# Kernel optimization log

Hardware: AMD Instinct MI355X
Metric: run time of the kernel (lower is better)

Reference implementation:

```python
import jax, jax.numpy as jnp
import numpy as np

H = 256
NUM_REL = 480
NUM_ENT = 23000
N_TRIPLES = 8192
T = 10  # cur_ts == path_len window


def _lin_params(key, din, dout):
    kw, _ = jax.random.split(key)
    W = jax.random.normal(kw, (din, dout), dtype=jnp.float32) * 0.02
    b = jnp.zeros((dout,), dtype=jnp.float32)
    return W, b


def setup_inputs() -> dict:
    key = jax.random.key(0)
    ks = jax.random.split(key, 16)
    pre_emb = jax.random.normal(ks[0], (NUM_ENT, H), dtype=jnp.float32)
    r_emb = jax.random.normal(ks[1], (NUM_REL, H), dtype=jnp.float32)
    # history counts: sparse non-negative (zeros are masked to -1e9 in softmax)
    part = jax.random.uniform(ks[2], (N_TRIPLES, T * NUM_REL), dtype=jnp.float32)
    mask = jax.random.uniform(ks[3], (N_TRIPLES, T * NUM_REL)) < 0.3
    partial_embeding = jnp.where(mask, part, 0.0)
    sub_idx = jax.random.randint(ks[4], (N_TRIPLES,), 0, NUM_ENT)
    rel_idx = jax.random.randint(ks[5], (N_TRIPLES,), 0, NUM_REL)
    obj_idx = jax.random.randint(ks[6], (N_TRIPLES,), 0, NUM_ENT)
    Wm1, bm1 = _lin_params(ks[7], H, 2 * H)
    Wm2, bm2 = _lin_params(ks[8], 2 * H, H)
    Wattn, battn = _lin_params(ks[9], H, H)
    Wh1, bh1 = _lin_params(ks[10], H, H)
    Wh2, bh2 = _lin_params(ks[11], H, H)
    Walign, balign = _lin_params(ks[12], H, H)
    Wih = jax.random.normal(ks[13], (H, 3 * H), dtype=jnp.float32) * 0.02
    Whh = jax.random.normal(ks[14], (H, 3 * H), dtype=jnp.float32) * 0.02
    bih = jnp.zeros((3 * H,), dtype=jnp.float32)
    bhh = jnp.zeros((3 * H,), dtype=jnp.float32)
    return dict(pre_emb=pre_emb, r_emb=r_emb, partial_embeding=partial_embeding,
                sub_idx=sub_idx, rel_idx=rel_idx, obj_idx=obj_idx, cur_ts=T,
                Wm1=Wm1, bm1=bm1, Wm2=Wm2, bm2=bm2, Wattn=Wattn, battn=battn,
                Wh1=Wh1, bh1=bh1, Wh2=Wh2, bh2=bh2, Walign=Walign, balign=balign,
                Wih=Wih, Whh=Whh, bih=bih, bhh=bhh)


def _gru_cell(x, h, Wih, Whh, bih, bhh):
    # torch.nn.GRUCell math
    gi = x @ Wih + bih
    gh = h @ Whh + bhh
    i_r, i_z, i_n = jnp.split(gi, 3, axis=-1)
    h_r, h_z, h_n = jnp.split(gh, 3, axis=-1)
    r = jax.nn.sigmoid(i_r + h_r)
    z = jax.nn.sigmoid(i_z + h_z)
    n = jnp.tanh(i_n + r * h_n)
    return (1.0 - z) * n + z * h


def reference(pre_emb, r_emb, partial_embeding, sub_idx, rel_idx, obj_idx, cur_ts,
              Wm1, bm1, Wm2, bm2, Wattn, battn, Wh1, bh1, Wh2, bh2,
              Walign, balign, Wih, Whh, bih, bhh):
    n = partial_embeding.shape[0]
    num_rel = r_emb.shape[0]
    t = cur_ts  # path window covers [0, cur_ts)
    # relation mapping
    mapped_rel = (r_emb @ Wm1 + bm1) @ Wm2 + bm2            # [R, H]
    q_rel = mapped_rel[rel_idx]                               # [N, H]
    # attention logits base (loop-invariant): q W_attn mapped_rel^T
    base = (q_rel @ Wattn + battn) @ mapped_rel.T            # [N, R]
    # [N, t*R] -> [t, N, R] time-major slices
    hist = partial_embeding[:, : t * num_rel].reshape(n, t, num_rel).swapaxes(0, 1)
    h0 = jnp.zeros((n, mapped_rel.shape[1]), dtype=pre_emb.dtype)

    def step(h, cur):
        attn = cur * base
        attn = jax.nn.softmax(jnp.where(attn == 0, -1e9, attn), axis=1)
        x = attn @ mapped_rel                                 # [N, H]
        return _gru_cell(x, h, Wih, Whh, bih, bhh), None

    gru_hidden, _ = jax.lax.scan(step, h0, hist)
    # predicted history + match loss
    predicted_hist = 0.1 * ((q_rel @ Wh1 + bh1) @ Wh2 + bh2) + q_rel
    match_loss = jnp.mean((predicted_hist - gru_hidden) ** 2)
    # forward_forth (distmult)
    h2 = _gru_cell(q_rel, predicted_hist, Wih, Whh, bih, bhh)  # [N, H]
    sub = pre_emb[sub_idx]
    score_ = ((sub @ Walign + balign) * h2) @ (pre_emb @ Walign + balign).T  # [N, E]
    # BCE(sigmoid(score_), one_hot(obj)): per-elem -y*logsig(s) - (1-y)*logsig(-s)
    pos = score_[jnp.arange(n), obj_idx]
    path_loss = (-jnp.sum(jax.nn.log_sigmoid(-score_)) - jnp.sum(pos)) / (score_.size)
    score = jax.nn.sigmoid(score_)
    return match_loss, path_loss, score
```

## Files before the change

kernel.cpp:

```cpp
#include <hip/hip_runtime.h>
#include <hip/hip_bf16.h>
#include <stdint.h>

#define DEV __device__ __forceinline__

typedef unsigned short u16;
typedef __attribute__((ext_vector_type(8))) short bf16x8;
typedef __attribute__((ext_vector_type(4))) float f32x4;
typedef __attribute__((ext_vector_type(4))) unsigned short u16x4;

constexpr int H  = 256;
constexpr int R  = 480;
constexpr int RP = 512;
constexpr int NE = 23000;
constexpr int NT = 8192;
constexpr int TT = 10;

DEV u16 f2b(float f) {
  union { float f; unsigned u; } x; x.f = f;
  unsigned u = x.u;
  return (u16)((u + 0x7fffu + ((u >> 16) & 1u)) >> 16);
}
DEV float b2f(u16 h) {
  union { unsigned u; float f; } x; x.u = ((unsigned)h) << 16;
  return x.f;
}

DEV void gload_lds16(const u16* g, u16* lds) {
  __builtin_amdgcn_global_load_lds(
      (const __attribute__((address_space(1))) unsigned int*)g,
      (__attribute__((address_space(3))) unsigned int*)lds, 16, 0, 0);
}

__launch_bounds__(256)
__global__ void stageA_k(const float* __restrict__ r_emb,
                         const float* __restrict__ Wm1, const float* __restrict__ bm1,
                         const float* __restrict__ Wm2, const float* __restrict__ bm2,
                         const float* __restrict__ Wattn, const float* __restrict__ battn,
                         const float* __restrict__ Wih,
                         const float* __restrict__ Wh1, const float* __restrict__ bh1,
                         const float* __restrict__ Wh2, const float* __restrict__ bh2,
                         const float* __restrict__ Whh, const float* __restrict__ bhh,
                         const float* __restrict__ bih, const float* __restrict__ Walign,
                         float* __restrict__ mapped, float* __restrict__ t1,
                         float* __restrict__ Pg, float* __restrict__ G2,
                         u16* __restrict__ MWT, u16* __restrict__ WhhT,
                         u16* __restrict__ WalignT, float* __restrict__ bsum) {
  const int j = threadIdx.x;
  if (blockIdx.x >= 480) {
    const int b = blockIdx.x - 480;
    if (b < 768) {
      WhhT[(size_t)b * 256 + j] = f2b(Whh[(size_t)j * 768 + b]);
    } else if (b < 1024) {
      const int n = b - 768;
      WalignT[(size_t)n * 256 + j] = f2b(Walign[(size_t)j * 256 + n]);
    } else if (b < 1027) {
      const int c = (b - 1024) * 256 + j;
      if (c < 768) bsum[c] = bih[c] + (c < 512 ? bhh[c] : 0.f);
    } else {
      const int row = (b - 1027) * 256 + j;
      if (row < 768) {
        const u16x4 z = {0, 0, 0, 0};
        #pragma unroll
        for (int c = 480; c < 512; c += 4) *(u16x4*)&MWT[(size_t)row * RP + c] = z;
      }
    }
    return;
  }
  __shared__ float re[256], hid[512], mp[256], p1l[256], Pl[256];
  __shared__ float mwl[768], pwl[768];
  __shared__ f32x4 red4[256];
  const int r = blockIdx.x;
  const f32x4 z4 = {0.f, 0.f, 0.f, 0.f};
  re[j] = r_emb[(size_t)r * 256 + j];
  __syncthreads();
  {
    const int q = j & 127, g = j >> 7;
    f32x4 acc = (g == 0) ? *(const f32x4*)&bm1[q * 4] : z4;
    for (int k = g * 128; k < g * 128 + 128; ++k)
      acc += re[k] * *(const f32x4*)&Wm1[(size_t)k * 512 + q * 4];
    red4[j] = acc;
    __syncthreads();
    if (j < 128) *(f32x4*)&hid[j * 4] = red4[j] + red4[j + 128];
    __syncthreads();
  }
  {
    const int q = j & 63, g = j >> 6;
    f32x4 acc = (g == 0) ? *(const f32x4*)&bm2[q * 4] : z4;
    for (int k = g * 128; k < g * 128 + 128; ++k)
      acc += hid[k] * *(const f32x4*)&Wm2[(size_t)k * 256 + q * 4];
    red4[j] = acc;
    __syncthreads();
    if (j < 64) {
      const f32x4 s = red4[j] + red4[j + 64] + red4[j + 128] + red4[j + 192];
      *(f32x4*)&mp[j * 4] = s;
      *(f32x4*)&mapped[(size_t)r * 256 + j * 4] = s;
    }
    __syncthreads();
  }
  {
    const int q = j & 63, g = j >> 6;
    f32x4 acc = (g == 0) ? *(const f32x4*)&battn[q * 4] : z4;
    for (int k = g * 64; k < g * 64 + 64; ++k)
      acc += mp[k] * *(const f32x4*)&Wattn[(size_t)k * 256 + q * 4];
    red4[j] = acc;
    __syncthreads();
    if (j < 64)
      *(f32x4*)&t1[(size_t)r * 256 + j * 4] =
          red4[j] + red4[j + 64] + red4[j + 128] + red4[j + 192];
    __syncthreads();
  }
  if (j < 192) {
    f32x4 acc = z4;
    for (int k = 0; k < 256; ++k)
      acc += mp[k] * *(const f32x4*)&Wih[(size_t)k * 768 + j * 4];
    *(f32x4*)&mwl[j * 4] = acc;
    #pragma unroll
    for (int c = 0; c < 4; ++c) MWT[(size_t)(j * 4 + c) * RP + r] = f2b(acc[c]);
  }
  __syncthreads();
  {
    const int q = j & 63, g = j >> 6;
    f32x4 acc = (g == 0) ? *(const f32x4*)&bh1[q * 4] : z4;
    for (int k = g * 64; k < g * 64 + 64; ++k)
      acc += mp[k] * *(const f32x4*)&Wh1[(size_t)k * 256 + q * 4];
    red4[j] = acc;
    __syncthreads();
    if (j < 64) *(f32x4*)&p1l[j * 4] = red4[j] + red4[j + 64] + red4[j + 128] + red4[j + 192];
    __syncthreads();
  }
  {
    const int q = j & 63, g = j >> 6;
    f32x4 acc = (g == 0) ? *(const f32x4*)&bh2[q * 4] : z4;
    for (int k = g * 64; k < g * 64 + 64; ++k)
      acc += p1l[k] * *(const f32x4*)&Wh2[(size_t)k * 256 + q * 4];
    red4[j] = acc;
    __syncthreads();
    if (j < 64) {
      f32x4 s = red4[j] + red4[j + 64] + red4[j + 128] + red4[j + 192];
      const f32x4 mv = *(const f32x4*)&mp[j * 4];
      #pragma unroll
      for (int c = 0; c < 4; ++c) s[c] = 0.1f * s[c] + mv[c];
      *(f32x4*)&Pl[j * 4] = s;
      *(f32x4*)&Pg[(size_t)r * 256 + j * 4] = s;
    }
    __syncthreads();
  }
  if (j < 192) {
    f32x4 acc = *(const f32x4*)&bhh[j * 4];
    for (int k = 0; k < 256; ++k)
      acc += Pl[k] * *(const f32x4*)&Whh[(size_t)k * 768 + j * 4];
    *(f32x4*)&pwl[j * 4] = acc;
  }
  __syncthreads();
  {
    const float rg = 1.f / (1.f + __expf(-(mwl[j] + bih[j] + pwl[j])));
    const float zg = 1.f / (1.f + __expf(-(mwl[j + 256] + bih[j + 256] + pwl[j + 256])));
    const float ng = tanhf(mwl[j + 512] + bih[j + 512] + rg * pwl[j + 512]);
    G2[(size_t)r * 256 + j] = (1.f - zg) * ng + zg * Pl[j];
  }
}

__global__ void sgemm_bt_k(const float* __restrict__ A, const float* __restrict__ W,
                           float* __restrict__ C, int M, int N, int K) {
  const int idx = blockIdx.x * 256 + threadIdx.x;
  if (idx >= M * N) return;
  const int i = idx / N, j = idx % N;
  const f32x4* a4 = (const f32x4*)(A + (size_t)i * K);
  const f32x4* w4 = (const f32x4*)(W + (size_t)j * K);
  f32x4 acc = {0.f, 0.f, 0.f, 0.f};
  for (int k = 0; k < K / 4; ++k) acc += a4[k] * w4[k];
  C[idx] = acc[0] + acc[1] + acc[2] + acc[3];
}

__global__ void softmax_all_k(const float* __restrict__ part, const float* __restrict__ B480,
                              const int* __restrict__ rel_idx, u16* __restrict__ attn) {
  const int task = blockIdx.x * 4 + (threadIdx.x >> 6);
  const int lane = threadIdx.x & 63;
  const int tt = task >> 13;
  const int i  = task & (NT - 1);
  const float* cur = part + (size_t)i * (TT * R) + (size_t)tt * R;
  const float* b = B480 + (size_t)rel_idx[i] * R;
  f32x4 v[2];
  float m = -3e38f;
  const bool act1 = lane < 56;
  #pragma unroll
  for (int jj = 0; jj < 2; ++jj) {
    const int r0 = jj * 256 + lane * 4;
    f32x4 val = {-1e9f, -1e9f, -1e9f, -1e9f};
    if (jj == 0 || act1) {
      const f32x4 c4 = *(const f32x4*)&cur[r0];
      const f32x4 b4 = *(const f32x4*)&b[r0];
      #pragma unroll
      for (int x = 0; x < 4; ++x) {
        val[x] = (c4[x] == 0.f) ? -1e9f : c4[x] * b4[x];
        m = fmaxf(m, val[x]);
      }
    }
    v[jj] = val;
  }
  #pragma unroll
  for (int o = 32; o; o >>= 1) m = fmaxf(m, __shfl_xor(m, o));
  float s = 0.f;
  #pragma unroll
  for (int jj = 0; jj < 2; ++jj) {
    if (jj == 0 || act1) {
      #pragma unroll
      for (int x = 0; x < 4; ++x) { v[jj][x] = __expf(v[jj][x] - m); s += v[jj][x]; }
    }
  }
  #pragma unroll
  for (int o = 32; o; o >>= 1) s += __shfl_xor(s, o);
  const float inv = 1.f / s;
  u16* arow = attn + (size_t)task * RP;
  #pragma unroll
  for (int jj = 0; jj < 2; ++jj) {
    const int r0 = jj * 256 + lane * 4;
    u16x4 o = {0, 0, 0, 0};
    if (jj == 0 || act1) {
      #pragma unroll
      for (int x = 0; x < 4; ++x) o[x] = f2b(v[jj][x] * inv);
    }
    *(u16x4*)&arow[r0] = o;
  }
}

__launch_bounds__(256)
__global__ void scan_k(const u16* __restrict__ WhhT, const float* __restrict__ bhh,
                       const u16* __restrict__ gi_all, float* __restrict__ hbuf) {
  __shared__ __align__(16) u16 As[32 * 256];
  __shared__ __align__(16) u16 Bs[2][192 * 64];
  const int tid = threadIdx.x;
  const int lane = tid & 63;
  const int wv = tid >> 6;
  const int rf = wv >> 1;
  const int ch = wv & 1;
  const int fr = lane & 15;
  const int fq = lane >> 4;
  const int row_l = rf * 16 + fr;
  const int grow = blockIdx.x * 32 + row_l;
  const int sw = (fr & 7) * 8;

  auto stageB = [&](int buf, int cg, int k0) {
    #pragma unroll
    for (int it = 0; it < 6; ++it) {
      const int c = it * 256 + tid;
      const int vr = c >> 3, s = c & 7;
      const int vcol = ((vr >> 6) * 256) + cg * 64 + (vr & 63);
      gload_lds16(WhhT + (size_t)vcol * 256 + k0 + ((s ^ (vr & 7)) * 8),
                  &Bs[buf][(it * 256 + wv * 64) * 8]);
    }
  };

  float hreg[4][2][4];
  #pragma unroll
  for (int cg = 0; cg < 4; ++cg)
    #pragma unroll
    for (int nn = 0; nn < 2; ++nn)
      #pragma unroll
      for (int j = 0; j < 4; ++j) hreg[cg][nn][j] = 0.f;

  for (int t = 0; t < TT; ++t) {
    const u16* gi = gi_all + (size_t)t * NT * 768;
    #pragma unroll
    for (int cg = 0; cg < 4; ++cg) {
      f32x4 acc[6] = {};
      u16x4 gv[3][2];
      #pragma unroll
      for (int nn = 0; nn < 2; ++nn) {
        const int c = cg * 64 + ch * 32 + nn * 16 + fq * 4;
        const size_t gb = (size_t)grow * 768 + c;
        gv[0][nn] = *(const u16x4*)&gi[gb];
        gv[1][nn] = *(const u16x4*)&gi[gb + 256];
        gv[2][nn] = *(const u16x4*)&gi[gb + 512];
      }
      if (t > 0) {
        stageB(0, cg, 0);
        #pragma unroll
        for (int ki = 0; ki < 4; ++ki) {
          const int cb = ki & 1;
          if (ki < 3) {
            stageB(cb ^ 1, cg, (ki + 1) * 64);
            asm volatile("s_waitcnt vmcnt(6)" ::: "memory");
          } else {
            asm volatile("s_waitcnt vmcnt(0)" ::: "memory");
          }
          __builtin_amdgcn_sched_barrier(0);
          __builtin_amdgcn_s_barrier();
          #pragma unroll
          for (int kk = 0; kk < 2; ++kk) {
            const int ko = (ki * 64 + kk * 32 + fq * 8) ^ sw;
            const bf16x8 a = *(const bf16x8*)&As[row_l * 256 + ko];
            const int bo = (kk * 32 + fq * 8) ^ sw;
            #pragma unroll
            for (int g = 0; g < 3; ++g)
              #pragma unroll
              for (int nn = 0; nn < 2; ++nn) {
                const int vr = g * 64 + ch * 32 + nn * 16 + fr;
                const bf16x8 b = *(const bf16x8*)&Bs[cb][vr * 64 + bo];
                acc[g * 2 + nn] =
                    __builtin_amdgcn_mfma_f32_16x16x32_bf16(b, a, acc[g * 2 + nn], 0, 0, 0);
              }
          }
          __builtin_amdgcn_s_barrier();
        }
      }
      #pragma unroll
      for (int nn = 0; nn < 2; ++nn) {
        const int c = cg * 64 + ch * 32 + nn * 16 + fq * 4;
        const f32x4 bn = *(const f32x4*)&bhh[512 + c];
        #pragma unroll
        for (int j = 0; j < 4; ++j) {
          const float rg = 1.f / (1.f + __expf(-(b2f(gv[0][nn][j]) + acc[nn][j])));
          const float zg = 1.f / (1.f + __expf(-(b2f(gv[1][nn][j]) + acc[2 + nn][j])));
          const float ng = tanhf(b2f(gv[2][nn][j]) + rg * (acc[4 + nn][j] + bn[j]));
          hreg[cg][nn][j] = (1.f - zg) * ng + zg * hreg[cg][nn][j];
        }
      }
    }
    #pragma unroll
    for (int cg = 0; cg < 4; ++cg)
      #pragma unroll
      for (int nn = 0; nn < 2; ++nn) {
        const int c = cg * 64 + ch * 32 + nn * 16 + fq * 4;
        u16x4 o;
        #pragma unroll
        for (int j = 0; j < 4; ++j) o[j] = f2b(hreg[cg][nn][j]);
        *(u16x4*)&As[row_l * 256 + (c ^ sw)] = o;
        if (t == TT - 1) {
          f32x4 hv;
          #pragma unroll
          for (int j = 0; j < 4; ++j) hv[j] = hreg[cg][nn][j];
          *(f32x4*)&hbuf[(size_t)grow * 256 + c] = hv;
        }
      }
    __syncthreads();
  }
}

__global__ void gather_sub_k(const float* __restrict__ pre, const int* __restrict__ sub,
                             u16* __restrict__ sb) {
  const int q = blockIdx.x * 256 + threadIdx.x;
  const int i = q >> 6, c = (q & 63) * 4;
  const f32x4 v = *(const f32x4*)&pre[(size_t)sub[i] * H + c];
  u16x4 o;
  #pragma unroll
  for (int j = 0; j < 4; ++j) o[j] = f2b(v[j]);
  *(u16x4*)&sb[(size_t)q * 4] = o;
}
__global__ void cvt_pre_k(const float* __restrict__ pre, u16* __restrict__ pb) {
  const int q = blockIdx.x * 256 + threadIdx.x;
  const f32x4 v = *(const f32x4*)&pre[(size_t)q * 4];
  u16x4 o;
  #pragma unroll
  for (int j = 0; j < 4; ++j) o[j] = f2b(v[j]);
  *(u16x4*)&pb[(size_t)q * 4] = o;
}

__global__ void finalize_k(const float* __restrict__ mp, const float* __restrict__ sp,
                           float* __restrict__ out) {
  const int tid = threadIdx.x;
  float s1 = 0.f, s2 = 0.f;
  for (int i = tid; i < 128; i += 256) s1 += mp[i];
  for (int i = tid; i < 2880; i += 256) s2 += sp[i];
  #pragma unroll
  for (int o = 32; o; o >>= 1) {
    s1 += __shfl_down(s1, o); s2 += __shfl_down(s2, o);
  }
  __shared__ float r1[4], r2[4];
  if ((tid & 63) == 0) { r1[tid >> 6] = s1; r2[tid >> 6] = s2; }
  __syncthreads();
  if (tid == 0) {
    const float a = r1[0] + r1[1] + r1[2] + r1[3];
    const float b = r2[0] + r2[1] + r2[2] + r2[3];
    out[0] = a / 2097152.f;
    out[1] = b / 188416000.f;
  }
}

template <int MODE>
__launch_bounds__(256)
__global__ void gemm_k(const u16* __restrict__ A, const u16* __restrict__ Bt,
                       const float* __restrict__ bias,
                       float* __restrict__ Cf, u16* __restrict__ Cb,
                       int M, int N, int K,
                       float* __restrict__ out2, float* __restrict__ part,
                       const int* __restrict__ idxv, const float* __restrict__ Pf,
                       const float* __restrict__ G2f, const float* __restrict__ hf) {
  __shared__ __align__(16) u16 As[128 * 64];
  __shared__ __align__(16) u16 Bs[128 * 64];
  __shared__ float red[4];
  const int tid = threadIdx.x;
  const int lane = tid & 63;
  const int wv = tid >> 6;
  const int nbx = gridDim.x;
  int flat = blockIdx.y * nbx + blockIdx.x;
  const int nwg = nbx * gridDim.y;
  if ((nwg & 7) == 0) flat = (flat & 7) * (nwg >> 3) + (flat >> 3);
  const int bx = flat % nbx;
  const int by = flat / nbx;
  const int m0 = by * 128;
  const int n0 = bx * 128;
  const int wm = (wv >> 1) * 64;
  const int wn = (wv & 1) * 64;
  const int fr = lane & 15;
  const int fq = lane >> 4;
  const int sw = (lane & 7) * 8;
  f32x4 acc[4][4] = {};

  const int nsteps = K >> 6;
  for (int kt = 0; kt < nsteps; ++kt) {
    const int k0 = kt * 64;
    if (kt > 0) __syncthreads();
    #pragma unroll
    for (int it = 0; it < 4; ++it) {
      const int c = it * 256 + tid;
      const int row = c >> 3, s = c & 7;
      const int sc = (s ^ (row & 7)) * 8;
      int gr = m0 + row; gr = gr < M ? gr : M - 1;
      gload_lds16(A + (size_t)gr * K + k0 + sc, &As[(it * 256 + wv * 64) * 8]);
      int nr = n0 + row; nr = nr < N ? nr : N - 1;
      gload_lds16(Bt + (size_t)nr * K + k0 + sc, &Bs[(it * 256 + wv * 64) * 8]);
    }
    asm volatile("s_waitcnt vmcnt(0)" ::: "memory");
    __builtin_amdgcn_sched_barrier(0);
    __builtin_amdgcn_s_barrier();
    #pragma unroll
    for (int kk = 0; kk < 2; ++kk) {
      const int ko = (kk * 32 + fq * 8) ^ sw;
      bf16x8 a[4], b[4];
      #pragma unroll
      for (int mi = 0; mi < 4; ++mi)
        a[mi] = *(const bf16x8*)&As[(wm + mi * 16 + fr) * 64 + ko];
      #pragma unroll
      for (int ni = 0; ni < 4; ++ni)
        b[ni] = *(const bf16x8*)&Bs[(wn + ni * 16 + fr) * 64 + ko];
      #pragma unroll
      for (int mi = 0; mi < 4; ++mi)
        #pragma unroll
        for (int ni = 0; ni < 4; ++ni)
          acc[mi][ni] = __builtin_amdgcn_mfma_f32_16x16x32_bf16(b[ni], a[mi], acc[mi][ni], 0, 0, 0);
    }
  }

  float local = 0.f;
  #pragma unroll
  for (int mi = 0; mi < 4; ++mi) {
    const int rowm = m0 + wm + mi * 16 + fr;
    int iv = 0;
    if (MODE == 2) iv = idxv[rowm < M ? rowm : M - 1];
    #pragma unroll
    for (int ni = 0; ni < 4; ++ni) {
      const int col = n0 + wn + ni * 16 + fq * 4;
      if (rowm < M && col < N) {
        f32x4 v = acc[mi][ni];
        if (MODE == 0) {
          if (bias != nullptr) {
            const f32x4 bv = *(const f32x4*)&bias[col];
            #pragma unroll
            for (int j = 0; j < 4; ++j) v[j] += bv[j];
          }
          if (Cf) *(f32x4*)&Cf[(size_t)rowm * N + col] = v;
          if (Cb) {
            u16x4 o;
            #pragma unroll
            for (int j = 0; j < 4; ++j) o[j] = f2b(v[j]);
            *(u16x4*)&Cb[(size_t)rowm * N + col] = o;
          }
        } else {
          const f32x4 bv = *(const f32x4*)&bias[col];
          const f32x4 Pv = *(const f32x4*)&Pf[(size_t)iv * H + col];
          const f32x4 Gv = *(const f32x4*)&G2f[(size_t)iv * H + col];
          const f32x4 hv = *(const f32x4*)&hf[(size_t)rowm * H + col];
          u16x4 o;
          #pragma unroll
          for (int j = 0; j < 4; ++j) {
            const float d = Pv[j] - hv[j];
            local += d * d;
            o[j] = f2b((v[j] + bv[j]) * Gv[j]);
          }
          *(u16x4*)&Cb[(size_t)rowm * N + col] = o;
        }
      }
    }
  }
  if (MODE == 2) {
    #pragma unroll
    for (int o = 32; o; o >>= 1) local += __shfl_down(local, o);
    if (lane == 0) red[wv] = local;
    __syncthreads();
    if (tid == 0) part[blockIdx.y * gridDim.x + blockIdx.x] = red[0] + red[1] + red[2] + red[3];
  }
}

template <int MODE>
__launch_bounds__(512)
__global__ void gemm256_k(const u16* __restrict__ A, const u16* __restrict__ Bt,
                          const float* __restrict__ bias, u16* __restrict__ Cb,
                          int M, int N, int K,
                          float* __restrict__ out2, float* __restrict__ part,
                          const int* __restrict__ idxv) {
  __shared__ __align__(16) u16 As[256 * 64];
  __shared__ __align__(16) u16 Bs[256 * 64];
  __shared__ float red[8];
  const int tid = threadIdx.x;
  const int lane = tid & 63;
  const int wv = tid >> 6;
  const int nbx = gridDim.x;
  int flat = blockIdx.y * nbx + blockIdx.x;
  const int nwg = nbx * gridDim.y;
  if ((nwg & 7) == 0) flat = (flat & 7) * (nwg >> 3) + (flat >> 3);
  const int bx = flat % nbx;
  const int by = flat / nbx;
  const int m0 = by * 256;
  const int n0 = bx * 256;
  const int wm = (wv >> 2) * 128;
  const int wn = (wv & 3) * 64;
  const int fr = lane & 15;
  const int fq = lane >> 4;
  const int sw = (lane & 7) * 8;
  f32x4 acc[8][4] = {};

  const int nsteps = K >> 6;
  for (int kt = 0; kt < nsteps; ++kt) {
    const int k0 = kt * 64;
    if (kt > 0) __syncthreads();
    #pragma unroll
    for (int it = 0; it < 4; ++it) {
      const int c = it * 512 + tid;
      const int row = c >> 3, s = c & 7;
      const int sc = (s ^ (row & 7)) * 8;
      int gr = m0 + row; gr = gr < M ? gr : M - 1;
      gload_lds16(A + (size_t)gr * K + k0 + sc, &As[(it * 512 + wv * 64) * 8]);
      int nr = n0 + row; nr = nr < N ? nr : N - 1;
      gload_lds16(Bt + (size_t)nr * K + k0 + sc, &Bs[(it * 512 + wv * 64) * 8]);
    }
    asm volatile("s_waitcnt vmcnt(0)" ::: "memory");
    __builtin_amdgcn_sched_barrier(0);
    __builtin_amdgcn_s_barrier();
    #pragma unroll
    for (int kk = 0; kk < 2; ++kk) {
      const int ko = (kk * 32 + fq * 8) ^ sw;
      bf16x8 a[8], b[4];
      #pragma unroll
      for (int mi = 0; mi < 8; ++mi)
        a[mi] = *(const bf16x8*)&As[(wm + mi * 16 + fr) * 64 + ko];
      #pragma unroll
      for (int ni = 0; ni < 4; ++ni)
        b[ni] = *(const bf16x8*)&Bs[(wn + ni * 16 + fr) * 64 + ko];
      #pragma unroll
      for (int mi = 0; mi < 8; ++mi)
        #pragma unroll
        for (int ni = 0; ni < 4; ++ni)
          acc[mi][ni] = __builtin_amdgcn_mfma_f32_16x16x32_bf16(b[ni], a[mi], acc[mi][ni], 0, 0, 0);
    }
  }

  float local = 0.f;
  #pragma unroll
  for (int mi = 0; mi < 8; ++mi) {
    const int rowm = m0 + wm + mi * 16 + fr;
    int iv = 0;
    if (MODE == 1) iv = idxv[rowm < M ? rowm : M - 1];
    #pragma unroll
    for (int ni = 0; ni < 4; ++ni) {
      const int col = n0 + wn + ni * 16 + fq * 4;
      if (rowm < M && col < N) {
        const f32x4 v = acc[mi][ni];
        if (MODE == 0) {
          const f32x4 bv = *(const f32x4*)&bias[col];
          u16x4 o;
          #pragma unroll
          for (int j = 0; j < 4; ++j) o[j] = f2b(v[j] + bv[j]);
          *(u16x4*)&Cb[(size_t)rowm * N + col] = o;
        } else {
          f32x4 sg;
          #pragma unroll
          for (int j = 0; j < 4; ++j) {
            const float s = v[j];
            const float sig = 1.f / (1.f + __expf(-s));
            sg[j] = sig;
            const float om = 1.f - sig;
            local += (om > 0.f) ? -__logf(om) : s;
            if (col + j == iv) local -= s;
          }
          *(f32x4*)&out2[(size_t)rowm * N + col] = sg;
        }
      }
    }
  }
  if (MODE == 1) {
    #pragma unroll
    for (int o = 32; o; o >>= 1) local += __shfl_down(local, o);
    if (lane == 0) red[wv] = local;
    __syncthreads();
    if (tid == 0) {
      float s = 0.f;
      #pragma unroll
      for (int x = 0; x < 8; ++x) s += red[x];
      part[blockIdx.y * gridDim.x + blockIdx.x] = s;
    }
  }
}

extern "C" void kernel_launch(void* const* d_in, const int* in_sizes, int n_in,
                              void* d_out, int out_size, void* d_ws, size_t ws_size,
                              hipStream_t stream) {
  const float* pre_emb = (const float*)d_in[0];
  const float* r_emb   = (const float*)d_in[1];
  const float* part_e  = (const float*)d_in[2];
  const int*   sub_idx = (const int*)d_in[3];
  const int*   rel_idx = (const int*)d_in[4];
  const int*   obj_idx = (const int*)d_in[5];
  const float* Wm1 = (const float*)d_in[7];  const float* bm1 = (const float*)d_in[8];
  const float* Wm2 = (const float*)d_in[9];  const float* bm2 = (const float*)d_in[10];
  const float* Wattn = (const float*)d_in[11]; const float* battn = (const float*)d_in[12];
  const float* Wh1 = (const float*)d_in[13]; const float* bh1 = (const float*)d_in[14];
  const float* Wh2 = (const float*)d_in[15]; const float* bh2 = (const float*)d_in[16];
  const float* Walign = (const float*)d_in[17]; const float* balign = (const float*)d_in[18];
  const float* Wih = (const float*)d_in[19]; const float* Whh = (const float*)d_in[20];
  const float* bih = (const float*)d_in[21]; const float* bhh = (const float*)d_in[22];
  float* out = (float*)d_out;

  char* w = (char*)d_ws;
  size_t off = 0;
  auto alloc = [&](size_t bytes) -> void* {
    off = (off + 255) & ~(size_t)255;
    void* p = w + off;
    off += bytes;
    return p;
  };
  float* mapped = (float*)alloc((size_t)R * H * 4);
  float* t1     = (float*)alloc((size_t)R * H * 4);
  float* B480   = (float*)alloc((size_t)R * R * 4);
  float* P      = (float*)alloc((size_t)R * H * 4);
  float* G2     = (float*)alloc((size_t)R * H * 4);
  u16* MWT      = (u16*)alloc((size_t)768 * RP * 2);
  u16* WhhT     = (u16*)alloc((size_t)768 * H * 2);
  u16* WalignT  = (u16*)alloc((size_t)H * H * 2);
  float* bsum   = (float*)alloc(768 * 4);
  float* hbuf   = (float*)alloc((size_t)NT * H * 4);
  u16* lhs_b    = (u16*)alloc((size_t)NT * H * 2);
  u16* sub_b    = (u16*)alloc((size_t)NT * H * 2);
  u16* pre_b    = (u16*)alloc((size_t)NE * H * 2);
  u16* alT      = (u16*)alloc((size_t)NE * H * 2);
  float* mpart  = (float*)alloc(128 * 4);
  float* spart  = (float*)alloc(2880 * 4);
  u16* attn_all = (u16*)alloc((size_t)TT * NT * RP * 2);
  u16* gi_all   = (u16*)alloc((size_t)TT * NT * 768 * 2);
  if (off > ws_size) return;

  stageA_k<<<480 + 1030, 256, 0, stream>>>(
      r_emb, Wm1, bm1, Wm2, bm2, Wattn, battn, Wih, Wh1, bh1, Wh2, bh2,
      Whh, bhh, bih, Walign, mapped, t1, P, G2, MWT, WhhT, WalignT, bsum);
  sgemm_bt_k<<<(R * R + 255) / 256, 256, 0, stream>>>(t1, mapped, B480, R, R, H);

  softmax_all_k<<<TT * (NT / 4), 256, 0, stream>>>(part_e, B480, rel_idx, attn_all);
  gemm256_k<0><<<dim3(3, TT * (NT / 256)), 512, 0, stream>>>(
      attn_all, MWT, bsum, gi_all, TT * NT, 768, RP, nullptr, nullptr, nullptr);
  scan_k<<<NT / 32, 256, 0, stream>>>(WhhT, bhh, gi_all, hbuf);

  gather_sub_k<<<NT / 4, 256, 0, stream>>>(pre_emb, sub_idx, sub_b);
  gemm_k<2><<<dim3(2, 64), 256, 0, stream>>>(
      sub_b, WalignT, balign, nullptr, lhs_b, NT, H, H,
      nullptr, mpart, rel_idx, P, G2, hbuf);

  cvt_pre_k<<<NE / 4, 256, 0, stream>>>(pre_emb, pre_b);
  gemm_k<0><<<dim3(2, 180), 256, 0, stream>>>(
      pre_b, WalignT, balign, nullptr, alT, NE, H, H,
      nullptr, nullptr, nullptr, nullptr, nullptr, nullptr);

  gemm256_k<1><<<dim3(90, 32), 512, 0, stream>>>(
      lhs_b, alT, nullptr, nullptr, NT, NE, H, out + 2, spart, obj_idx);

  finalize_k<<<1, 256, 0, stream>>>(mpart, spart, out);
}
```

Baseline: 1.077 ms.

## Replace final score GEMM with full-K single-load 128x128 tile kernel

The final N×E scoring GEMM with the sigmoid/BCE epilogue moves from the 256x256, 512-thread templated kernel to a dedicated 128x128, 256-thread kernel. The new kernel loads the whole K=256 slice of A and B into LDS once with XOR-swizzled direct-to-LDS loads and runs a single MFMA pass, so the K loop and its repeated barriers go away. It also remaps blocks so each XCD gets a contiguous range of column tiles, using a padded grid where the excess blocks write zero partials. The trade-offs are 128 KB of LDS per block, which limits occupancy, and four times as many partial sums for the finalize kernel to reduce.

```diff
diff --git a/kernel.cpp b/kernel.cpp
--- a/kernel.cpp
+++ b/kernel.cpp
@@ -362,7 +362,7 @@
   const int tid = threadIdx.x;
   float s1 = 0.f, s2 = 0.f;
   for (int i = tid; i < 128; i += 256) s1 += mp[i];
-  for (int i = tid; i < 2880; i += 256) s2 += sp[i];
+  for (int i = tid; i < 11776; i += 256) s2 += sp[i];
   #pragma unroll
   for (int o = 32; o; o >>= 1) {
     s1 += __shfl_down(s1, o); s2 += __shfl_down(s2, o);
@@ -493,16 +493,12 @@
   }
 }
 
-template <int MODE>
 __launch_bounds__(512)
 __global__ void gemm256_k(const u16* __restrict__ A, const u16* __restrict__ Bt,
                           const float* __restrict__ bias, u16* __restrict__ Cb,
-                          int M, int N, int K,
-                          float* __restrict__ out2, float* __restrict__ part,
-                          const int* __restrict__ idxv) {
+                          int M, int N, int K) {
   __shared__ __align__(16) u16 As[256 * 64];
   __shared__ __align__(16) u16 Bs[256 * 64];
-  __shared__ float red[8];
   const int tid = threadIdx.x;
   const int lane = tid & 63;
   const int wv = tid >> 6;
@@ -556,51 +552,118 @@
     }
   }
 
-  float local = 0.f;
   #pragma unroll
   for (int mi = 0; mi < 8; ++mi) {
     const int rowm = m0 + wm + mi * 16 + fr;
-    int iv = 0;
-    if (MODE == 1) iv = idxv[rowm < M ? rowm : M - 1];
     #pragma unroll
     for (int ni = 0; ni < 4; ++ni) {
       const int col = n0 + wn + ni * 16 + fq * 4;
       if (rowm < M && col < N) {
         const f32x4 v = acc[mi][ni];
-        if (MODE == 0) {
-          const f32x4 bv = *(const f32x4*)&bias[col];
-          u16x4 o;
-          #pragma unroll
-          for (int j = 0; j < 4; ++j) o[j] = f2b(v[j] + bv[j]);
-          *(u16x4*)&Cb[(size_t)rowm * N + col] = o;
-        } else {
-          f32x4 sg;
-          #pragma unroll
-          for (int j = 0; j < 4; ++j) {
-            const float s = v[j];
-            const float sig = 1.f / (1.f + __expf(-s));
-            sg[j] = sig;
-            const float om = 1.f - sig;
-            local += (om > 0.f) ? -__logf(om) : s;
-            if (col + j == iv) local -= s;
-          }
-          *(f32x4*)&out2[(size_t)rowm * N + col] = sg;
+        const f32x4 bv = *(const f32x4*)&bias[col];
+        u16x4 o;
+        #pragma unroll
+        for (int j = 0; j < 4; ++j) o[j] = f2b(v[j] + bv[j]);
+        *(u16x4*)&Cb[(size_t)rowm * N + col] = o;
+      }
+    }
+  }
+}
+
+__launch_bounds__(256)
+__global__ void gemmFK_k(const u16* __restrict__ A, const u16* __restrict__ Bt,
+                         float* __restrict__ out2, float* __restrict__ part,
+                         const int* __restrict__ idxv) {
+  __shared__ __align__(16) u16 As[128 * 256];
+  __shared__ __align__(16) u16 Bs[128 * 256];
+  __shared__ float red[4];
+  constexpr int N = NE;
+  constexpr int K = 256;
+  const int tid = threadIdx.x;
+  const int lane = tid & 63;
+  const int wv = tid >> 6;
+  const int flat = blockIdx.y * 184 + blockIdx.x;
+  const int pslot = flat;
+  const int xcd = flat & 7;
+  const int idx = flat >> 3;
+  const int bx = xcd * 23 + (idx % 23);
+  const int by = idx / 23;
+  if (bx >= 180) {
+    if (tid == 0) part[pslot] = 0.f;
+    return;
+  }
+  const int m0 = by * 128;
+  const int n0 = bx * 128;
+  const int wm = (wv >> 1) * 64;
+  const int wn = (wv & 1) * 64;
+  const int fr = lane & 15;
+  const int fq = lane >> 4;
+
+  #pragma unroll
+  for (int it = 0; it < 16; ++it) {
+    const int c = it * 256 + tid;
+    const int row = c >> 5, s = c & 31;
+    const int sc = (s ^ (row & 7)) * 8;
+    const int gr = m0 + row;
+    gload_lds16(A + (size_t)gr * K + sc, &As[(it * 256 + wv * 64) * 8]);
+    int nr = n0 + row; nr = nr < N ? nr : N - 1;
+    gload_lds16(Bt + (size_t)nr * K + sc, &Bs[(it * 256 + wv * 64) * 8]);
+  }
+  asm volatile("s_waitcnt vmcnt(0)" ::: "memory");
+  __builtin_amdgcn_sched_barrier(0);
+  __builtin_amdgcn_s_barrier();
+
+  f32x4 acc[4][4] = {};
+  #pragma unroll
+  for (int ksl = 0; ksl < 8; ++ksl) {
+    bf16x8 a[4], b[4];
+    #pragma unroll
+    for (int mi = 0; mi < 4; ++mi) {
+      const int row = wm + mi * 16 + fr;
+      const int slot = (ksl * 4 + fq) ^ (row & 7);
+      a[mi] = *(const bf16x8*)&As[row * 256 + slot * 8];
+    }
+    #pragma unroll
+    for (int ni = 0; ni < 4; ++ni) {
+      const int row = wn + ni * 16 + fr;
+      const int slot = (ksl * 4 + fq) ^ (row & 7);
+      b[ni] = *(const bf16x8*)&Bs[row * 256 + slot * 8];
+    }
+    #pragma unroll
+    for (int mi = 0; mi < 4; ++mi)
+      #pragma unroll
+      for (int ni = 0; ni < 4; ++ni)
+        acc[mi][ni] = __builtin_amdgcn_mfma_f32_16x16x32_bf16(b[ni], a[mi], acc[mi][ni], 0, 0, 0);
+  }
+
+  float local = 0.f;
+  #pragma unroll
+  for (int mi = 0; mi < 4; ++mi) {
+    const int rowm = m0 + wm + mi * 16 + fr;
+    const int iv = idxv[rowm];
+    #pragma unroll
+    for (int ni = 0; ni < 4; ++ni) {
+      const int col = n0 + wn + ni * 16 + fq * 4;
+      if (col < N) {
+        f32x4 sg;
+        #pragma unroll
+        for (int j = 0; j < 4; ++j) {
+          const float s = acc[mi][ni][j];
+          const float sig = 1.f / (1.f + __expf(-s));
+          sg[j] = sig;
+          const float om = 1.f - sig;
+          local += (om > 0.f) ? -__logf(om) : s;
+          if (col + j == iv) local -= s;
         }
-      }
-    }
-  }
-  if (MODE == 1) {
-    #pragma unroll
-    for (int o = 32; o; o >>= 1) local += __shfl_down(local, o);
-    if (lane == 0) red[wv] = local;
-    __syncthreads();
-    if (tid == 0) {
-      float s = 0.f;
-      #pragma unroll
-      for (int x = 0; x < 8; ++x) s += red[x];
-      part[blockIdx.y * gridDim.x + blockIdx.x] = s;
-    }
-  }
+        *(f32x4*)&out2[(size_t)rowm * N + col] = sg;
+      }
+    }
+  }
+  #pragma unroll
+  for (int o = 32; o; o >>= 1) local += __shfl_down(local, o);
+  if (lane == 0) red[wv] = local;
+  __syncthreads();
+  if (tid == 0) part[pslot] = red[0] + red[1] + red[2] + red[3];
 }
 
 extern "C" void kernel_launch(void* const* d_in, const int* in_sizes, int n_in,
@@ -645,7 +708,7 @@
   u16* pre_b    = (u16*)alloc((size_t)NE * H * 2);
   u16* alT      = (u16*)alloc((size_t)NE * H * 2);
   float* mpart  = (float*)alloc(128 * 4);
-  float* spart  = (float*)alloc(2880 * 4);
+  float* spart  = (float*)alloc(11776 * 4);
   u16* attn_all = (u16*)alloc((size_t)TT * NT * RP * 2);
   u16* gi_all   = (u16*)alloc((size_t)TT * NT * 768 * 2);
   if (off > ws_size) return;
@@ -656,8 +719,8 @@
   sgemm_bt_k<<<(R * R + 255) / 256, 256, 0, stream>>>(t1, mapped, B480, R, R, H);
 
   softmax_all_k<<<TT * (NT / 4), 256, 0, stream>>>(part_e, B480, rel_idx, attn_all);
-  gemm256_k<0><<<dim3(3, TT * (NT / 256)), 512, 0, stream>>>(
-      attn_all, MWT, bsum, gi_all, TT * NT, 768, RP, nullptr, nullptr, nullptr);
+  gemm256_k<<<dim3(3, TT * (NT / 256)), 512, 0, stream>>>(
+      attn_all, MWT, bsum, gi_all, TT * NT, 768, RP);
   scan_k<<<NT / 32, 256, 0, stream>>>(WhhT, bhh, gi_all, hbuf);
 
   gather_sub_k<<<NT / 4, 256, 0, stream>>>(pre_emb, sub_idx, sub_b);
@@ -670,8 +733,7 @@
       pre_b, WalignT, balign, nullptr, alT, NE, H, H,
       nullptr, nullptr, nullptr, nullptr, nullptr, nullptr);
 
-  gemm256_k<1><<<dim3(90, 32), 512, 0, stream>>>(
-      lhs_b, alT, nullptr, nullptr, NT, NE, H, out + 2, spart, obj_idx);
+  gemmFK_k<<<dim3(184, 64), 256, 0, stream>>>(lhs_b, alT, out + 2, spart, obj_idx);
 
   finalize_k<<<1, 256, 0, stream>>>(mpart, spart, out);
 }
```

After: 1.171 ms. 8.8% more time.
